# Performance work log

Measured on AMD Instinct MI355X. Metric: run time of the kernel, lower is better.

The kernel has to match this reference:

```python
import jax, jax.numpy as jnp
import numpy as np

N = 1_000_000        # nodes (contact_net.size()[0])
N_EDGES = 32_000_000  # nnz of contact_net (avg degree 32)


def setup_inputs() -> dict:
    key = jax.random.key(0)
    k1, k2, k3, k4, k5, k6, k7 = jax.random.split(key, 7)
    # Epidemic state E: inf => susceptible, <=1 => infective (relu(E-1)==0), >1 => exposed
    u = jax.random.uniform(k1, (N,))
    E = jnp.where(u < 0.5, jnp.inf, jnp.where(u < 0.8, 0.5, 5.0)).astype(jnp.float32)
    susceptiveness = jax.random.uniform(k2, (N,), dtype=jnp.float32)
    infectiveness = jax.random.uniform(k3, (N,), dtype=jnp.float32) * 0.1  # keep 1 - s*i > 0
    incubation = jax.random.uniform(k4, (N,), dtype=jnp.float32) * 14.0 + 1.0
    rand_vals = jax.random.uniform(k5, (N,), dtype=jnp.float32)  # replaces torch.rand(n)
    src = jax.random.randint(k6, (N_EDGES,), 0, N, dtype=jnp.int64 if jax.config.jax_enable_x64 else jnp.int32)
    dst = jax.random.randint(k7, (N_EDGES,), 0, N, dtype=src.dtype if True else jnp.int32)
    return dict(E=E, susceptiveness=susceptiveness, infectiveness=infectiveness,
                incubation=incubation, rand_vals=rand_vals, src=src, dst=dst)


def reference(E, susceptiveness, infectiveness, incubation, rand_vals, src, dst):
    # E = relu(E - 1)
    E = jax.nn.relu(E - 1.0)
    # infective mask (no infective_name given) and susceptible mask
    infective = (E == 0.0).astype(E.dtype) * infectiveness        # [N]
    susceptible = (E == jnp.inf).astype(E.dtype) * susceptiveness  # [N]
    # per-edge gather -> log(1 - p_edge)
    vals = jnp.log(1.0 - susceptible[src] * infective[dst])        # [N_EDGES]
    # sparse mm with ones vector == row-wise segment sum over src
    row_logp = jax.ops.segment_sum(vals, src, num_segments=N)      # [N]
    dI_prob = 1.0 - jnp.exp(row_logp)                              # [N]
    dI = rand_vals < dI_prob                                       # Bernoulli sample
    E_new = jnp.where(dI, incubation, E)
    return E_new
```

## Files before the change

### kernel.cpp

```cpp
#include <hip/hip_runtime.h>
#include <hip/hip_fp16.h>
#include <math.h>
#include <float.h>


typedef int v4i __attribute__((ext_vector_type(4)));

#define MAX_BIT_WORDS 32768

__global__ void prep_full(const float* __restrict__ E,
                          const float* __restrict__ susc,
                          const float* __restrict__ infc,
                          __half* __restrict__ sus,
                          __half* __restrict__ infv,
                          unsigned long long* __restrict__ gbits,
                          float* __restrict__ acc,
                          int n) {
    int i = blockIdx.x * blockDim.x + threadIdx.x;
    float e = (i < n) ? E[i] : 2.0f;
    bool infective = (i < n) && (e <= 1.0f);
    unsigned long long m = __ballot(infective);
    if (i < n) {
        sus[i]  = __float2half(isinf(e) ? susc[i] : 0.0f);
        infv[i] = __float2half(infective ? infc[i] : 0.0f);
        acc[i]  = 0.0f;
    }
    if (gbits && (threadIdx.x & 63) == 0 && i < n) {
        gbits[i >> 6] = m;
    }
}

__global__ void prep_acc_only(float* __restrict__ acc, int n) {
    int i = blockIdx.x * blockDim.x + threadIdx.x;
    if (i < n) acc[i] = 0.0f;
}

__global__ __launch_bounds__(1024, 4) void edge_lds(
        const int* __restrict__ src,
        const int* __restrict__ dst,
        const __half* __restrict__ sus,
        const __half* __restrict__ infv,
        const unsigned int* __restrict__ gbits,
        float* __restrict__ acc,
        int n_edges, int nwords) {
    __shared__ unsigned int bits[MAX_BIT_WORDS];
    for (int w = threadIdx.x; w < nwords; w += 1024)
        bits[w] = gbits[w];
    __syncthreads();

    const unsigned short* susu  = (const unsigned short*)sus;
    const unsigned short* infvu = (const unsigned short*)infv;

    long long nchunk = (long long)n_edges >> 3;
    long long stride = (long long)gridDim.x * blockDim.x;
    for (long long c = (long long)blockIdx.x * blockDim.x + threadIdx.x;
         c < nchunk; c += stride) {
        v4i s0 = __builtin_nontemporal_load((const v4i*)src + 2 * c);
        v4i s1 = __builtin_nontemporal_load((const v4i*)src + 2 * c + 1);
        v4i d0 = __builtin_nontemporal_load((const v4i*)dst + 2 * c);
        v4i d1 = __builtin_nontemporal_load((const v4i*)dst + 2 * c + 1);
        int ss[8] = {s0.x, s0.y, s0.z, s0.w, s1.x, s1.y, s1.z, s1.w};
        int dd[8] = {d0.x, d0.y, d0.z, d0.w, d1.x, d1.y, d1.z, d1.w};
#pragma unroll
        for (int k = 0; k < 8; ++k) {
            int d = dd[k];
            if ((bits[d >> 5] >> (d & 31)) & 1u) {
                int s = ss[k];
                unsigned short svu = susu[s];
                if (svu) {
                    float sv = __half2float(__ushort_as_half(svu));
                    float iv = __half2float(__ushort_as_half(infvu[d]));
                    float p = sv * iv;
                    if (p != 0.0f)
                        atomicAdd(&acc[s], __log2f(1.0f - p));
                }
            }
        }
    }

    long long tb = nchunk << 3;
    int tail = (int)(n_edges - tb);
    if (blockIdx.x == 0 && (int)threadIdx.x < tail) {
        long long e = tb + threadIdx.x;
        int d = dst[e];
        if ((bits[d >> 5] >> (d & 31)) & 1u) {
            int s = src[e];
            unsigned short svu = susu[s];
            if (svu) {
                float sv = __half2float(__ushort_as_half(svu));
                float iv = __half2float(__ushort_as_half(infvu[d]));
                float p = sv * iv;
                if (p != 0.0f)
                    atomicAdd(&acc[s], __log2f(1.0f - p));
            }
        }
    }
}

__global__ void edge_fast(const int* __restrict__ src,
                          const int* __restrict__ dst,
                          const __half* __restrict__ sus,
                          const __half* __restrict__ infv,
                          float* __restrict__ acc,
                          int n_edges) {
    int t = blockIdx.x * blockDim.x + threadIdx.x;
    long long base = (long long)t * 4;
    if (base + 3 < n_edges) {
        v4i s4 = __builtin_nontemporal_load((const v4i*)src + t);
        v4i d4 = __builtin_nontemporal_load((const v4i*)dst + t);
        int ss[4] = {s4.x, s4.y, s4.z, s4.w};
        int dd[4] = {d4.x, d4.y, d4.z, d4.w};
#pragma unroll
        for (int k = 0; k < 4; ++k) {
            float sv = __half2float(sus[ss[k]]);
            if (sv != 0.0f) {
                float iv = __half2float(infv[dd[k]]);
                if (iv != 0.0f) {
                    atomicAdd(&acc[ss[k]], __log2f(1.0f - sv * iv));
                }
            }
        }
    } else if (base < n_edges) {
        for (long long e = base; e < n_edges; ++e) {
            int s = src[e];
            float sv = __half2float(sus[s]);
            if (sv != 0.0f) {
                float iv = __half2float(infv[dst[e]]);
                if (iv != 0.0f) atomicAdd(&acc[s], __log2f(1.0f - sv * iv));
            }
        }
    }
}

__global__ void edge_inline(const int* __restrict__ src,
                            const int* __restrict__ dst,
                            const float* __restrict__ E,
                            const float* __restrict__ susc,
                            const float* __restrict__ infc,
                            float* __restrict__ acc,
                            int n_edges) {
    long long e = (long long)blockIdx.x * blockDim.x + threadIdx.x;
    if (e < n_edges) {
        int s = src[e];
        if (isinf(E[s])) {
            int d = dst[e];
            if (E[d] <= 1.0f) {
                atomicAdd(&acc[s], __log2f(1.0f - susc[s] * infc[d]));
            }
        }
    }
}

__global__ void final_kernel(const float* __restrict__ E,
                             const float* __restrict__ rnd,
                             const float* __restrict__ incub,
                             float* __restrict__ out,
                             int n) {
    int i = blockIdx.x * blockDim.x + threadIdx.x;
    if (i < n) {
        float a = out[i];
        float e_new = fmaxf(E[i] - 1.0f, 0.0f);
        float p = 1.0f - exp2f(a);
        float r = (rnd[i] < p) ? incub[i] : e_new;
        unsigned bits = __float_as_uint(r);
        if ((bits & 0x7f800000u) == 0x7f800000u) r = 3.0e38f;
        out[i] = r;
    }
}

extern "C" void kernel_launch(void* const* d_in, const int* in_sizes, int n_in,
                              void* d_out, int out_size, void* d_ws, size_t ws_size,
                              hipStream_t stream) {
    const float* E     = (const float*)d_in[0];
    const float* susc  = (const float*)d_in[1];
    const float* infc  = (const float*)d_in[2];
    const float* incub = (const float*)d_in[3];
    const float* rnd   = (const float*)d_in[4];
    const int*   src   = (const int*)d_in[5];
    const int*   dst   = (const int*)d_in[6];
    int n       = in_sizes[0];
    int n_edges = in_sizes[5];

    float* acc = (float*)d_out;

    const int B = 256;
    int nb_nodes = (n + B - 1) / B;

    int nwords64 = (n + 63) / 64;
    int nwords32 = (n + 31) / 32;
    size_t tables_bytes = (size_t)4 * n;
    size_t bits_off     = (tables_bytes + 7) & ~(size_t)7;
    size_t need_lds     = bits_off + (size_t)nwords64 * 8;

    if (ws_size >= need_lds && nwords32 <= MAX_BIT_WORDS) {
        __half* sus  = (__half*)d_ws;
        __half* infv = sus + n;
        unsigned long long* gbits = (unsigned long long*)((char*)d_ws + bits_off);
        prep_full<<<nb_nodes, B, 0, stream>>>(E, susc, infc, sus, infv, gbits, acc, n);
        edge_lds<<<256, 1024, 0, stream>>>(src, dst, sus, infv,
                                           (const unsigned int*)gbits, acc,
                                           n_edges, nwords32);
    } else if (ws_size >= tables_bytes) {
        __half* sus  = (__half*)d_ws;
        __half* infv = sus + n;
        prep_full<<<nb_nodes, B, 0, stream>>>(E, susc, infc, sus, infv, nullptr, acc, n);
        int n_vec = (n_edges + 3) / 4;
        edge_fast<<<(n_vec + B - 1) / B, B, 0, stream>>>(src, dst, sus, infv, acc, n_edges);
    } else {
        prep_acc_only<<<nb_nodes, B, 0, stream>>>(acc, n);
        long long nb_e = ((long long)n_edges + B - 1) / B;
        edge_inline<<<(unsigned)nb_e, B, 0, stream>>>(src, dst, E, susc, infc, acc, n_edges);
    }

    final_kernel<<<nb_nodes, B, 0, stream>>>(E, rnd, incub, acc, n);
}
```

Before: 488.1 us.

## Software-pipeline edge loads with 16 edges per thread and branchless gathers

The edge kernel now handles 16 edges per thread per iteration and prefetches the next chunk's src/dst vectors while the current chunk is processed. The per-edge nested branches are replaced by staged, predicated gathers: all bitmask tests first, then all susceptibility loads (redirected to index 0 when masked), then all infectiveness loads, then the atomics. This is meant to raise memory-level parallelism and hide the latency of the streaming loads and random gathers. It costs more registers per thread under the 1024x4 launch bounds, which may cause spills or lower occupancy, and it issues a gather for every edge even when the mask rejects it.

After: 513.5 us. 1.05x slower.

```diff
diff --git a/kernel.cpp b/kernel.cpp
--- a/kernel.cpp
+++ b/kernel.cpp
@@ -7,6 +7,7 @@
 typedef int v4i __attribute__((ext_vector_type(4)));
 
 #define MAX_BIT_WORDS 32768
+#define EPT 16
 
 __global__ void prep_full(const float* __restrict__ E,
                           const float* __restrict__ susc,
@@ -51,43 +52,77 @@
     const unsigned short* susu  = (const unsigned short*)sus;
     const unsigned short* infvu = (const unsigned short*)infv;
 
-    long long nchunk = (long long)n_edges >> 3;
+    long long nchunk = (long long)n_edges / EPT;
     long long stride = (long long)gridDim.x * blockDim.x;
-    for (long long c = (long long)blockIdx.x * blockDim.x + threadIdx.x;
-         c < nchunk; c += stride) {
-        v4i s0 = __builtin_nontemporal_load((const v4i*)src + 2 * c);
-        v4i s1 = __builtin_nontemporal_load((const v4i*)src + 2 * c + 1);
-        v4i d0 = __builtin_nontemporal_load((const v4i*)dst + 2 * c);
-        v4i d1 = __builtin_nontemporal_load((const v4i*)dst + 2 * c + 1);
-        int ss[8] = {s0.x, s0.y, s0.z, s0.w, s1.x, s1.y, s1.z, s1.w};
-        int dd[8] = {d0.x, d0.y, d0.z, d0.w, d1.x, d1.y, d1.z, d1.w};
-#pragma unroll
-        for (int k = 0; k < 8; ++k) {
-            int d = dd[k];
-            if ((bits[d >> 5] >> (d & 31)) & 1u) {
-                int s = ss[k];
-                unsigned short svu = susu[s];
-                if (svu) {
-                    float sv = __half2float(__ushort_as_half(svu));
-                    float iv = __half2float(__ushort_as_half(infvu[d]));
-                    float p = sv * iv;
-                    if (p != 0.0f)
-                        atomicAdd(&acc[s], __log2f(1.0f - p));
-                }
-            }
-        }
-    }
-
-    long long tb = nchunk << 3;
+    long long c = (long long)blockIdx.x * blockDim.x + threadIdx.x;
+
+    if (c < nchunk) {
+        v4i s4[4], d4[4];
+#pragma unroll
+        for (int q = 0; q < 4; ++q) {
+            s4[q] = __builtin_nontemporal_load((const v4i*)src + 4 * c + q);
+            d4[q] = __builtin_nontemporal_load((const v4i*)dst + 4 * c + q);
+        }
+        for (;;) {
+            long long cn = c + stride;
+            bool have_next = cn < nchunk;
+            long long cp = have_next ? cn : c;
+            v4i s4n[4], d4n[4];
+#pragma unroll
+            for (int q = 0; q < 4; ++q) {
+                s4n[q] = __builtin_nontemporal_load((const v4i*)src + 4 * cp + q);
+                d4n[q] = __builtin_nontemporal_load((const v4i*)dst + 4 * cp + q);
+            }
+
+            int ss[EPT], dd[EPT];
+#pragma unroll
+            for (int q = 0; q < 4; ++q) {
+                ss[4*q+0] = s4[q].x; ss[4*q+1] = s4[q].y; ss[4*q+2] = s4[q].z; ss[4*q+3] = s4[q].w;
+                dd[4*q+0] = d4[q].x; dd[4*q+1] = d4[q].y; dd[4*q+2] = d4[q].z; dd[4*q+3] = d4[q].w;
+            }
+
+            bool pass[EPT];
+#pragma unroll
+            for (int k = 0; k < EPT; ++k)
+                pass[k] = (bits[dd[k] >> 5] >> (dd[k] & 31)) & 1u;
+
+            unsigned short svu[EPT];
+#pragma unroll
+            for (int k = 0; k < EPT; ++k)
+                svu[k] = susu[pass[k] ? ss[k] : 0];
+
+            unsigned short ivu[EPT];
+#pragma unroll
+            for (int k = 0; k < EPT; ++k) {
+                bool p2 = pass[k] && (svu[k] != 0);
+                ivu[k] = infvu[p2 ? dd[k] : 0];
+            }
+
+#pragma unroll
+            for (int k = 0; k < EPT; ++k) {
+                float sv = pass[k] ? __half2float(__ushort_as_half(svu[k])) : 0.0f;
+                float p  = sv * __half2float(__ushort_as_half(ivu[k]));
+                if (p != 0.0f)
+                    atomicAdd(&acc[ss[k]], __log2f(1.0f - p));
+            }
+
+            if (!have_next) break;
+            c = cn;
+#pragma unroll
+            for (int q = 0; q < 4; ++q) { s4[q] = s4n[q]; d4[q] = d4n[q]; }
+        }
+    }
+
+    long long tb = nchunk * EPT;
     int tail = (int)(n_edges - tb);
     if (blockIdx.x == 0 && (int)threadIdx.x < tail) {
         long long e = tb + threadIdx.x;
         int d = dst[e];
         if ((bits[d >> 5] >> (d & 31)) & 1u) {
             int s = src[e];
-            unsigned short svu = susu[s];
-            if (svu) {
-                float sv = __half2float(__ushort_as_half(svu));
+            unsigned short svu0 = susu[s];
+            if (svu0) {
+                float sv = __half2float(__ushort_as_half(svu0));
                 float iv = __half2float(__ushort_as_half(infvu[d]));
                 float p = sv * iv;
                 if (p != 0.0f)
```

## Split edge pass into compaction filter and dense processing kernel

Applied to the files above, without the earlier changes.

Replaces the single edge kernel with a two-phase scheme. The first kernel streams src/dst, tests the destination's infective bit in LDS, and compacts surviving (src,dst) pairs into a workspace buffer using wave scans and one global atomic per block. A second kernel then runs the gathers and atomics over the compacted list. The aim is to separate streaming from divergent random gathers so each phase keeps full occupancy. In exchange it writes and rereads about 30% of the edges as 8-byte pairs, adds a launch and block-level syncs, and only runs when the workspace is large enough (n_edges/3 pairs).

Result: slower. 564.5 us (+15.6%).

```diff
diff --git a/kernel.cpp b/kernel.cpp
--- a/kernel.cpp
+++ b/kernel.cpp
@@ -14,6 +14,7 @@
                           __half* __restrict__ sus,
                           __half* __restrict__ infv,
                           unsigned long long* __restrict__ gbits,
+                          unsigned int* __restrict__ gctr,
                           float* __restrict__ acc,
                           int n) {
     int i = blockIdx.x * blockDim.x + threadIdx.x;
@@ -28,11 +29,174 @@
     if (gbits && (threadIdx.x & 63) == 0 && i < n) {
         gbits[i >> 6] = m;
     }
+    if (gctr && blockIdx.x == 0 && threadIdx.x == 0) *gctr = 0;
 }
 
 __global__ void prep_acc_only(float* __restrict__ acc, int n) {
     int i = blockIdx.x * blockDim.x + threadIdx.x;
     if (i < n) acc[i] = 0.0f;
+}
+
+__global__ __launch_bounds__(1024, 4) void edge_filter(
+        const int* __restrict__ src,
+        const int* __restrict__ dst,
+        const unsigned int* __restrict__ gbits,
+        const unsigned short* __restrict__ susu,
+        const unsigned short* __restrict__ infvu,
+        float* __restrict__ acc,
+        unsigned long long* __restrict__ pairs,
+        unsigned int* __restrict__ gctr,
+        unsigned int capacity,
+        int n_edges, int nwords) {
+    __shared__ unsigned int bits[MAX_BIT_WORDS];
+    __shared__ unsigned int wave_cnt[16];
+    __shared__ unsigned int wave_base[16];
+    for (int w = threadIdx.x; w < nwords; w += 1024)
+        bits[w] = gbits[w];
+    __syncthreads();
+
+    const int lane = threadIdx.x & 63;
+    const int wid  = threadIdx.x >> 6;
+
+    long long nchunk = (long long)n_edges >> 3;
+    long long stride = (long long)gridDim.x * blockDim.x;
+
+    for (long long cb = (long long)blockIdx.x * blockDim.x; cb < nchunk; cb += stride) {
+        long long c = cb + threadIdx.x;
+        bool active = c < nchunk;
+
+        int ss[8], dd[8];
+        unsigned pm = 0;
+        if (active) {
+            v4i s0 = __builtin_nontemporal_load((const v4i*)src + 2 * c);
+            v4i s1 = __builtin_nontemporal_load((const v4i*)src + 2 * c + 1);
+            v4i d0 = __builtin_nontemporal_load((const v4i*)dst + 2 * c);
+            v4i d1 = __builtin_nontemporal_load((const v4i*)dst + 2 * c + 1);
+            ss[0]=s0.x; ss[1]=s0.y; ss[2]=s0.z; ss[3]=s0.w;
+            ss[4]=s1.x; ss[5]=s1.y; ss[6]=s1.z; ss[7]=s1.w;
+            dd[0]=d0.x; dd[1]=d0.y; dd[2]=d0.z; dd[3]=d0.w;
+            dd[4]=d1.x; dd[5]=d1.y; dd[6]=d1.z; dd[7]=d1.w;
+#pragma unroll
+            for (int k = 0; k < 8; ++k)
+                pm |= ((bits[dd[k] >> 5] >> (dd[k] & 31)) & 1u) << k;
+        }
+        int cnt = __popc(pm);
+
+        int scan = cnt;
+#pragma unroll
+        for (int off = 1; off < 64; off <<= 1) {
+            int v = __shfl_up(scan, off, 64);
+            if (lane >= off) scan += v;
+        }
+        if (lane == 63) wave_cnt[wid] = (unsigned)scan;
+        __syncthreads();
+        if (threadIdx.x == 0) {
+            unsigned run = 0;
+#pragma unroll
+            for (int w = 0; w < 16; ++w) { unsigned t = wave_cnt[w]; wave_cnt[w] = run; run += t; }
+            unsigned base = run ? atomicAdd(gctr, run) : 0u;
+#pragma unroll
+            for (int w = 0; w < 16; ++w) wave_base[w] = base + wave_cnt[w];
+        }
+        __syncthreads();
+
+        unsigned mybase = wave_base[wid] + (unsigned)(scan - cnt);
+#pragma unroll
+        for (int k = 0; k < 8; ++k) {
+            if (pm & (1u << k)) {
+                unsigned pos = mybase + (unsigned)__popc(pm & ((1u << k) - 1));
+                if (pos < capacity) {
+                    pairs[pos] = ((unsigned long long)(unsigned)dd[k] << 32)
+                               | (unsigned long long)(unsigned)ss[k];
+                } else {
+                    unsigned short svu = susu[ss[k]];
+                    if (svu) {
+                        float sv = __half2float(__ushort_as_half(svu));
+                        float iv = __half2float(__ushort_as_half(infvu[dd[k]]));
+                        float p = sv * iv;
+                        if (p != 0.0f) atomicAdd(&acc[ss[k]], __log2f(1.0f - p));
+                    }
+                }
+            }
+        }
+    }
+
+    long long tb = nchunk << 3;
+    int tail = (int)(n_edges - tb);
+    if (blockIdx.x == 0 && (int)threadIdx.x < tail) {
+        long long e = tb + threadIdx.x;
+        int d = dst[e];
+        if ((bits[d >> 5] >> (d & 31)) & 1u) {
+            int s = src[e];
+            unsigned short svu = susu[s];
+            if (svu) {
+                float sv = __half2float(__ushort_as_half(svu));
+                float iv = __half2float(__ushort_as_half(infvu[d]));
+                float p = sv * iv;
+                if (p != 0.0f) atomicAdd(&acc[s], __log2f(1.0f - p));
+            }
+        }
+    }
+}
+
+__global__ __launch_bounds__(256) void edge_process(
+        const unsigned long long* __restrict__ pairs,
+        const unsigned int* __restrict__ gctr,
+        const unsigned short* __restrict__ susu,
+        const unsigned short* __restrict__ infvu,
+        float* __restrict__ acc,
+        unsigned int capacity) {
+    unsigned int m = *gctr;
+    if (m > capacity) m = capacity;
+    long long stride4 = (long long)gridDim.x * blockDim.x * 4;
+    for (long long b = ((long long)blockIdx.x * blockDim.x + threadIdx.x) * 4;
+         b < (long long)m; b += stride4) {
+        unsigned long long p0, p1, p2, p3;
+        bool w1, w2, w3;
+        if (b + 3 < (long long)m) {
+            const v4i* vp = (const v4i*)(pairs + b);
+            v4i q0 = vp[0], q1 = vp[1];
+            p0 = ((unsigned long long)(unsigned)q0.y << 32) | (unsigned)q0.x;
+            p1 = ((unsigned long long)(unsigned)q0.w << 32) | (unsigned)q0.z;
+            p2 = ((unsigned long long)(unsigned)q1.y << 32) | (unsigned)q1.x;
+            p3 = ((unsigned long long)(unsigned)q1.w << 32) | (unsigned)q1.z;
+            w1 = w2 = w3 = true;
+        } else {
+            w1 = b + 1 < (long long)m;
+            w2 = b + 2 < (long long)m;
+            w3 = b + 3 < (long long)m;
+            p0 = pairs[b];
+            p1 = w1 ? pairs[b + 1] : 0ull;
+            p2 = w2 ? pairs[b + 2] : 0ull;
+            p3 = w3 ? pairs[b + 3] : 0ull;
+        }
+        int s0 = (int)(p0 & 0xffffffffu), d0 = (int)(p0 >> 32);
+        int s1 = (int)(p1 & 0xffffffffu), d1 = (int)(p1 >> 32);
+        int s2 = (int)(p2 & 0xffffffffu), d2 = (int)(p2 >> 32);
+        int s3 = (int)(p3 & 0xffffffffu), d3 = (int)(p3 >> 32);
+
+        unsigned short a0 = susu[s0];
+        unsigned short a1 = susu[s1];
+        unsigned short a2 = susu[s2];
+        unsigned short a3 = susu[s3];
+        if (!w1) a1 = 0;
+        if (!w2) a2 = 0;
+        if (!w3) a3 = 0;
+
+        unsigned short i0 = infvu[a0 ? d0 : 0];
+        unsigned short i1 = infvu[a1 ? d1 : 0];
+        unsigned short i2 = infvu[a2 ? d2 : 0];
+        unsigned short i3 = infvu[a3 ? d3 : 0];
+
+        float pr0 = __half2float(__ushort_as_half(a0)) * __half2float(__ushort_as_half(i0));
+        float pr1 = __half2float(__ushort_as_half(a1)) * __half2float(__ushort_as_half(i1));
+        float pr2 = __half2float(__ushort_as_half(a2)) * __half2float(__ushort_as_half(i2));
+        float pr3 = __half2float(__ushort_as_half(a3)) * __half2float(__ushort_as_half(i3));
+        if (pr0 != 0.0f) atomicAdd(&acc[s0], __log2f(1.0f - pr0));
+        if (pr1 != 0.0f) atomicAdd(&acc[s1], __log2f(1.0f - pr1));
+        if (pr2 != 0.0f) atomicAdd(&acc[s2], __log2f(1.0f - pr2));
+        if (pr3 != 0.0f) atomicAdd(&acc[s3], __log2f(1.0f - pr3));
+    }
 }
 
 __global__ __launch_bounds__(1024, 4) void edge_lds(
@@ -190,20 +354,44 @@
     int nwords32 = (n + 31) / 32;
     size_t tables_bytes = (size_t)4 * n;
     size_t bits_off     = (tables_bytes + 7) & ~(size_t)7;
-    size_t need_lds     = bits_off + (size_t)nwords64 * 8;
-
-    if (ws_size >= need_lds && nwords32 <= MAX_BIT_WORDS) {
+    size_t ctr_off      = bits_off + (size_t)nwords64 * 8;
+    size_t pairs_off    = (ctr_off + 8 + 15) & ~(size_t)15;
+    size_t need_lds     = ctr_off;
+
+    size_t cap_avail = (ws_size > pairs_off) ? (ws_size - pairs_off) / 8 : 0;
+    size_t cap_need  = (size_t)n_edges / 3 + 65536;
+    if (cap_avail > (size_t)n_edges) cap_avail = (size_t)n_edges;
+
+    if (nwords32 <= MAX_BIT_WORDS && cap_avail >= cap_need) {
         __half* sus  = (__half*)d_ws;
         __half* infv = sus + n;
         unsigned long long* gbits = (unsigned long long*)((char*)d_ws + bits_off);
-        prep_full<<<nb_nodes, B, 0, stream>>>(E, susc, infc, sus, infv, gbits, acc, n);
+        unsigned int* gctr = (unsigned int*)((char*)d_ws + ctr_off);
+        unsigned long long* pairs = (unsigned long long*)((char*)d_ws + pairs_off);
+        unsigned int capacity = (unsigned int)cap_avail;
+
+        prep_full<<<nb_nodes, B, 0, stream>>>(E, susc, infc, sus, infv, gbits, gctr, acc, n);
+        edge_filter<<<256, 1024, 0, stream>>>(src, dst, (const unsigned int*)gbits,
+                                              (const unsigned short*)sus,
+                                              (const unsigned short*)infv,
+                                              acc, pairs, gctr, capacity,
+                                              n_edges, nwords32);
+        edge_process<<<2048, 256, 0, stream>>>(pairs, gctr,
+                                               (const unsigned short*)sus,
+                                               (const unsigned short*)infv,
+                                               acc, capacity);
+    } else if (ws_size >= need_lds && nwords32 <= MAX_BIT_WORDS) {
+        __half* sus  = (__half*)d_ws;
+        __half* infv = sus + n;
+        unsigned long long* gbits = (unsigned long long*)((char*)d_ws + bits_off);
+        prep_full<<<nb_nodes, B, 0, stream>>>(E, susc, infc, sus, infv, gbits, nullptr, acc, n);
         edge_lds<<<256, 1024, 0, stream>>>(src, dst, sus, infv,
                                            (const unsigned int*)gbits, acc,
                                            n_edges, nwords32);
     } else if (ws_size >= tables_bytes) {
         __half* sus  = (__half*)d_ws;
         __half* infv = sus + n;
-        prep_full<<<nb_nodes, B, 0, stream>>>(E, susc, infc, sus, infv, nullptr, acc, n);
+        prep_full<<<nb_nodes, B, 0, stream>>>(E, susc, infc, sus, infv, nullptr, nullptr, acc, n);
         int n_vec = (n_edges + 3) / 4;
         edge_fast<<<(n_vec + B - 1) / B, B, 0, stream>>>(src, dst, sus, infv, acc, n_edges);
     } else {
```

## Bin infective edges by source bucket and accumulate in LDS per bucket

Applied to the files above, without the earlier changes.

Adds a two-pass scheme. The first pass filters edges whose destination is infective and writes packed (local src, dst) records into per-block, per-bucket regions sized by the available workspace. The second pass has each block handle one 4096-node bucket, keeping susceptibility and accumulators in shared memory and using LDS atomics instead of random global atomics. Records that overflow a region fall back to direct global atomics. The cost is extra global writes and reads of the binned records, and a 20-bit dst field that limits n to about one million nodes.

After: 745.2 us. 1.53x slower.

```diff
diff --git a/kernel.cpp b/kernel.cpp
--- a/kernel.cpp
+++ b/kernel.cpp
@@ -7,6 +7,9 @@
 typedef int v4i __attribute__((ext_vector_type(4)));
 
 #define MAX_BIT_WORDS 32768
+#define NBLK1 256
+#define BUCKET_SHIFT 12
+#define BUCKET_SIZE 4096
 
 __global__ void prep_full(const float* __restrict__ E,
                           const float* __restrict__ susc,
@@ -33,6 +36,133 @@
 __global__ void prep_acc_only(float* __restrict__ acc, int n) {
     int i = blockIdx.x * blockDim.x + threadIdx.x;
     if (i < n) acc[i] = 0.0f;
+}
+
+__global__ __launch_bounds__(1024, 4) void edge_bin(
+        const int* __restrict__ src,
+        const int* __restrict__ dst,
+        const unsigned int* __restrict__ gbits,
+        const unsigned short* __restrict__ susu,
+        const unsigned short* __restrict__ infvu,
+        float* __restrict__ acc,
+        unsigned int* __restrict__ regions,
+        unsigned int* __restrict__ bcounts,
+        int n_edges, int nwords, int nbuck, int rcap) {
+    __shared__ unsigned int bits[MAX_BIT_WORDS];
+    __shared__ unsigned int bcnt[NBLK1];
+    for (int w = threadIdx.x; w < nwords; w += 1024)
+        bits[w] = gbits[w];
+    if (threadIdx.x < (unsigned)nbuck) bcnt[threadIdx.x] = 0;
+    __syncthreads();
+
+    const long long region_base = (long long)blockIdx.x * nbuck * rcap;
+
+    long long nchunk = (long long)n_edges >> 3;
+    long long stride = (long long)gridDim.x * blockDim.x;
+    for (long long c = (long long)blockIdx.x * blockDim.x + threadIdx.x;
+         c < nchunk; c += stride) {
+        v4i s0 = __builtin_nontemporal_load((const v4i*)src + 2 * c);
+        v4i s1 = __builtin_nontemporal_load((const v4i*)src + 2 * c + 1);
+        v4i d0 = __builtin_nontemporal_load((const v4i*)dst + 2 * c);
+        v4i d1 = __builtin_nontemporal_load((const v4i*)dst + 2 * c + 1);
+        int ss[8] = {s0.x, s0.y, s0.z, s0.w, s1.x, s1.y, s1.z, s1.w};
+        int dd[8] = {d0.x, d0.y, d0.z, d0.w, d1.x, d1.y, d1.z, d1.w};
+#pragma unroll
+        for (int k = 0; k < 8; ++k) {
+            int d = dd[k];
+            if ((bits[d >> 5] >> (d & 31)) & 1u) {
+                int s = ss[k];
+                int b = s >> BUCKET_SHIFT;
+                unsigned rec = ((unsigned)(s & (BUCKET_SIZE - 1)) << 20) | (unsigned)d;
+                unsigned pos = atomicAdd(&bcnt[b], 1u);
+                if (pos < (unsigned)rcap) {
+                    __builtin_nontemporal_store(rec,
+                        regions + region_base + (long long)b * rcap + pos);
+                } else {
+                    unsigned short svu = susu[s];
+                    if (svu) {
+                        float sv = __half2float(__ushort_as_half(svu));
+                        float iv = __half2float(__ushort_as_half(infvu[d]));
+                        float p = sv * iv;
+                        if (p != 0.0f) atomicAdd(&acc[s], __log2f(1.0f - p));
+                    }
+                }
+            }
+        }
+    }
+
+    __syncthreads();
+    if (threadIdx.x < (unsigned)nbuck) {
+        bcounts[blockIdx.x * nbuck + threadIdx.x] = bcnt[threadIdx.x];
+    }
+
+    long long tb = nchunk << 3;
+    int tail = (int)(n_edges - tb);
+    if (blockIdx.x == 0 && (int)threadIdx.x < tail) {
+        long long e = tb + threadIdx.x;
+        int d = dst[e];
+        if ((bits[d >> 5] >> (d & 31)) & 1u) {
+            int s = src[e];
+            unsigned short svu = susu[s];
+            if (svu) {
+                float sv = __half2float(__ushort_as_half(svu));
+                float iv = __half2float(__ushort_as_half(infvu[d]));
+                float p = sv * iv;
+                if (p != 0.0f) atomicAdd(&acc[s], __log2f(1.0f - p));
+            }
+        }
+    }
+}
+
+__global__ __launch_bounds__(1024, 4) void bucket_process(
+        const unsigned int* __restrict__ regions,
+        const unsigned int* __restrict__ bcounts,
+        const unsigned short* __restrict__ susu,
+        const unsigned short* __restrict__ infvu,
+        float* __restrict__ acc,
+        int n, int nbuck, int rcap) {
+    __shared__ unsigned short lsus[BUCKET_SIZE];
+    __shared__ float laccs[BUCKET_SIZE];
+
+    const int b = blockIdx.x;
+    const int base_node = b << BUCKET_SHIFT;
+
+    for (int i = threadIdx.x; i < BUCKET_SIZE; i += blockDim.x) {
+        int g = base_node + i;
+        lsus[i]  = (g < n) ? susu[g] : (unsigned short)0;
+        laccs[i] = 0.0f;
+    }
+    __syncthreads();
+
+    const int wid  = threadIdx.x >> 6;
+    const int lane = threadIdx.x & 63;
+    const int nw   = blockDim.x >> 6;
+
+    for (int blk = wid; blk < NBLK1; blk += nw) {
+        unsigned cnt = bcounts[blk * nbuck + b];
+        if (cnt > (unsigned)rcap) cnt = (unsigned)rcap;
+        const long long rb = ((long long)blk * nbuck + b) * (long long)rcap;
+        for (unsigned i = lane; i < cnt; i += 64) {
+            unsigned rec = __builtin_nontemporal_load(regions + rb + i);
+            int sl = (int)(rec >> 20);
+            int d  = (int)(rec & 0xFFFFFu);
+            unsigned short svu = lsus[sl];
+            unsigned short ivu = infvu[svu ? d : 0];
+            float p = __half2float(__ushort_as_half(svu)) *
+                      __half2float(__ushort_as_half(ivu));
+            if (p != 0.0f)
+                atomicAdd(&laccs[sl], __log2f(1.0f - p));
+        }
+    }
+    __syncthreads();
+
+    for (int i = threadIdx.x; i < BUCKET_SIZE; i += blockDim.x) {
+        int g = base_node + i;
+        if (g < n) {
+            float v = laccs[i];
+            if (v != 0.0f) acc[g] += v;
+        }
+    }
 }
 
 __global__ __launch_bounds__(1024, 4) void edge_lds(
@@ -188,11 +318,40 @@
 
     int nwords64 = (n + 63) / 64;
     int nwords32 = (n + 31) / 32;
+    int nbuck    = (n + BUCKET_SIZE - 1) >> BUCKET_SHIFT;
+
     size_t tables_bytes = (size_t)4 * n;
     size_t bits_off     = (tables_bytes + 7) & ~(size_t)7;
-    size_t need_lds     = bits_off + (size_t)nwords64 * 8;
-
-    if (ws_size >= need_lds && nwords32 <= MAX_BIT_WORDS) {
+    size_t bcounts_off  = bits_off + (size_t)nwords64 * 8;
+    size_t regions_off  = (bcounts_off + (size_t)NBLK1 * nbuck * 4 + 15) & ~(size_t)15;
+
+    long long rcap = 0;
+    if (ws_size > regions_off) {
+        size_t avail = ws_size - regions_off;
+        rcap = (long long)(avail / ((size_t)NBLK1 * (size_t)nbuck * 4));
+        if (rcap > 512) rcap = 512;
+    }
+
+    size_t need_r6 = bcounts_off;
+
+    if (nwords32 <= MAX_BIT_WORDS && nbuck <= NBLK1 && rcap >= 224) {
+        __half* sus  = (__half*)d_ws;
+        __half* infv = sus + n;
+        unsigned long long* gbits = (unsigned long long*)((char*)d_ws + bits_off);
+        unsigned int* bcounts = (unsigned int*)((char*)d_ws + bcounts_off);
+        unsigned int* regions = (unsigned int*)((char*)d_ws + regions_off);
+
+        prep_full<<<nb_nodes, B, 0, stream>>>(E, susc, infc, sus, infv, gbits, acc, n);
+        edge_bin<<<NBLK1, 1024, 0, stream>>>(src, dst, (const unsigned int*)gbits,
+                                             (const unsigned short*)sus,
+                                             (const unsigned short*)infv,
+                                             acc, regions, bcounts,
+                                             n_edges, nwords32, nbuck, (int)rcap);
+        bucket_process<<<nbuck, 1024, 0, stream>>>(regions, bcounts,
+                                                   (const unsigned short*)sus,
+                                                   (const unsigned short*)infv,
+                                                   acc, n, nbuck, (int)rcap);
+    } else if (ws_size >= need_r6 && nwords32 <= MAX_BIT_WORDS) {
         __half* sus  = (__half*)d_ws;
         __half* infv = sus + n;
         unsigned long long* gbits = (unsigned long long*)((char*)d_ws + bits_off);
```
